# Kernel tuning notes

Measured on AMD Instinct MI355X. Metric: run time of the kernel, lower is better.

## Reference

```python
import jax, jax.numpy as jnp
import numpy as np

ROUTINGS = 3
NUM_CAPSULE = 32
DIM_CAPSULE = 64


def squash(x, axis=-1):
    # scale = sqrt(||x||^2 + eps) / (0.5 + ||x||^2 + eps)
    sq = jnp.sum(x * x, axis=axis, keepdims=True) + 1e-7
    return (jnp.sqrt(sq) / (0.5 + sq)) * x


def setup_inputs() -> dict:
    key = jax.random.key(0)
    k1, k2 = jax.random.split(key)
    B, IN, ID = 64, 1024, 256
    u_vecs = jax.random.normal(k1, (B, IN, ID), dtype=jnp.float32)
    # nn.Linear weight [NC*DC, ID], xavier_normal init
    fan_out, fan_in = NUM_CAPSULE * DIM_CAPSULE, ID
    std = np.sqrt(2.0 / (fan_in + fan_out)).astype(np.float32)
    W = jax.random.normal(k2, (fan_out, fan_in), dtype=jnp.float32) * std
    return {"u_vecs": u_vecs, "W": W}


def reference(u_vecs, W):
    B, IN, ID = u_vecs.shape
    # Linear projection: [B, IN, NC*DC]
    u_hat = jnp.einsum('bid,od->bio', u_vecs, W)
    # -> [B, NC, IN, DC]
    u_hat = u_hat.reshape(B, IN, NUM_CAPSULE, DIM_CAPSULE).transpose(0, 2, 1, 3)

    b = jnp.zeros((B, NUM_CAPSULE, IN), dtype=u_hat.dtype)
    o = None
    for i in range(ROUTINGS):
        c = jax.nn.softmax(b, axis=1)                      # softmax over output capsules
        o = jnp.einsum('bni,bnid->bnd', c, u_hat)          # [B, NC, DC]
        if i < ROUTINGS - 1:
            # F.normalize(o, 2, -1): x / max(||x||, 1e-12)
            norm = jnp.linalg.norm(o, axis=-1, keepdims=True)
            o = o / jnp.maximum(norm, 1e-12)
            b = jnp.einsum('bnid,bnd->bni', u_hat, o)
    return squash(o)
```

## Files before the change

### kernel.cpp

```cpp
#include <hip/hip_runtime.h>
#include <math.h>


#define B   64
#define IN  1024
#define ID  256
#define NC  32
#define DC  64

__global__ __launch_bounds__(256) void k_sumu(const float* __restrict__ u,
                                              float* __restrict__ sp0) {
    const int c = blockIdx.x, b = blockIdx.y;
    const int d = threadIdx.x;
    const float* up = u + ((size_t)b * IN + (size_t)c * (IN / 8)) * ID + d;
    float acc = 0.f;
#pragma unroll 8
    for (int i = 0; i < IN / 8; ++i) acc += up[(size_t)i * ID];
    sp0[(c * B + b) * ID + d] = acc;
}

__global__ __launch_bounds__(256) void k_ot(const float* __restrict__ W,
                                            const float* __restrict__ src,
                                            float* __restrict__ tout,
                                            const int mode) {
    const int bn = blockIdx.x;
    const int b = bn / NC, n = bn % NC;
    __shared__ float s_lds[ID];
    __shared__ float o_lds[DC];
    __shared__ float on_lds[DC];
    const int tid = threadIdx.x;

    float sv = 0.f;
    if (mode == 0) {
#pragma unroll
        for (int c = 0; c < 8; ++c) sv += src[(c * B + b) * ID + tid];
        sv *= (1.0f / NC);
    } else {
#pragma unroll
        for (int c = 0; c < 8; ++c) sv += src[((size_t)(c * B + b) * NC + n) * ID + tid];
    }
    s_lds[tid] = sv;
    __syncthreads();

    const int wave = tid >> 6, lane = tid & 63;
    const float* Wn = W + (size_t)n * DC * ID;
#pragma unroll 4
    for (int r = 0; r < 16; ++r) {
        const int d = wave * 16 + r;
        const float* wrow = Wn + (size_t)d * ID;
        float p = wrow[lane]        * s_lds[lane]
                + wrow[lane + 64]   * s_lds[lane + 64]
                + wrow[lane + 128]  * s_lds[lane + 128]
                + wrow[lane + 192]  * s_lds[lane + 192];
#pragma unroll
        for (int off = 32; off > 0; off >>= 1) p += __shfl_down(p, off);
        if (lane == 0) o_lds[d] = p;
    }
    __syncthreads();

    if (mode == 2) {
        if (tid < DC) {
            float v = o_lds[tid];
            float sq = v * v;
#pragma unroll
            for (int off = 32; off > 0; off >>= 1) sq += __shfl_down(sq, off);
            sq = __shfl(sq, 0) + 1e-7f;
            const float sc = sqrtf(sq) / (0.5f + sq);
            tout[(size_t)(b * NC + n) * DC + tid] = v * sc;
        }
        return;
    }

    if (tid < DC) {
        float v = o_lds[tid];
        float sq = v * v;
#pragma unroll
        for (int off = 32; off > 0; off >>= 1) sq += __shfl_down(sq, off);
        sq = __shfl(sq, 0);
        const float inv = 1.0f / fmaxf(sqrtf(sq), 1e-12f);
        on_lds[tid] = v * inv;
    }
    __syncthreads();

    float acc = 0.f;
    const float* wc = Wn + tid;
#pragma unroll 8
    for (int d = 0; d < DC; ++d) acc += wc[(size_t)d * ID] * on_lds[d];
    tout[((size_t)b * NC + n) * ID + tid] = acc;
}

#define RTILE 128
__global__ __launch_bounds__(512) void k_route(const float* __restrict__ u,
                                               const float* __restrict__ t,
                                               float* __restrict__ sp) {
    const int it = blockIdx.x, b = blockIdx.y;
    const int iBase = it * RTILE;
    __shared__ float Tc[16][36];
    __shared__ float Us[16][132];
    __shared__ float cl[RTILE][36];
    const int tid = threadIdx.x;

    const int q = tid >> 3;
    const int r = tid & 7;
    float acc[2][4] = {{0.f}};
    const float* ub = u + ((size_t)b * IN + iBase) * ID;
    const float* tb = t + (size_t)b * NC * ID;
    const int tn = tid >> 4, tk = tid & 15;

    for (int kc = 0; kc < ID / 16; ++kc) {
        __syncthreads();
        {
            const int i = tid >> 2, c4 = tid & 3;
            const float4 v = *(const float4*)(ub + (size_t)i * ID + kc * 16 + c4 * 4);
            Us[c4 * 4 + 0][i] = v.x;
            Us[c4 * 4 + 1][i] = v.y;
            Us[c4 * 4 + 2][i] = v.z;
            Us[c4 * 4 + 3][i] = v.w;
        }
        Tc[tk][tn] = tb[(size_t)tn * ID + kc * 16 + tk];
        __syncthreads();
#pragma unroll
        for (int k = 0; k < 16; ++k) {
            const float2 a2 = *(const float2*)&Us[k][q * 2];
            const float4 b4 = *(const float4*)&Tc[k][r * 4];
            const float av[2] = {a2.x, a2.y};
            const float bv[4] = {b4.x, b4.y, b4.z, b4.w};
#pragma unroll
            for (int ii = 0; ii < 2; ++ii)
#pragma unroll
                for (int jj = 0; jj < 4; ++jj) acc[ii][jj] += av[ii] * bv[jj];
        }
    }

#pragma unroll
    for (int ii = 0; ii < 2; ++ii)
        *(float4*)&cl[q * 2 + ii][r * 4] =
            make_float4(acc[ii][0], acc[ii][1], acc[ii][2], acc[ii][3]);
    __syncthreads();

    {
        const int i = tid >> 2, quad = tid & 3;
        float v[8];
#pragma unroll
        for (int j = 0; j < 8; ++j) v[j] = cl[i][quad * 8 + j];
        float mx = v[0];
#pragma unroll
        for (int j = 1; j < 8; ++j) mx = fmaxf(mx, v[j]);
        mx = fmaxf(mx, __shfl_xor(mx, 1));
        mx = fmaxf(mx, __shfl_xor(mx, 2));
        float sum = 0.f;
#pragma unroll
        for (int j = 0; j < 8; ++j) { v[j] = __expf(v[j] - mx); sum += v[j]; }
        sum += __shfl_xor(sum, 1);
        sum += __shfl_xor(sum, 2);
        const float inv = 1.0f / sum;
#pragma unroll
        for (int j = 0; j < 8; ++j) cl[i][quad * 8 + j] = v[j] * inv;
    }
    __syncthreads();

    const int d4 = tid & 63;
    const int ng = tid >> 6;
    float a2[4][4] = {{0.f}};
    const float* ur = ub + d4 * 4;
#pragma unroll 4
    for (int i = 0; i < RTILE; ++i) {
        const float4 uv = *(const float4*)(ur + (size_t)i * ID);
        const float4 c0 = *(const float4*)&cl[i][ng * 4];
        const float cv[4] = {c0.x, c0.y, c0.z, c0.w};
        const float uvv[4] = {uv.x, uv.y, uv.z, uv.w};
#pragma unroll
        for (int j = 0; j < 4; ++j)
#pragma unroll
            for (int x = 0; x < 4; ++x) a2[j][x] += cv[j] * uvv[x];
    }

    float* spb = sp + (size_t)(it * B + b) * NC * ID;
#pragma unroll
    for (int j = 0; j < 4; ++j) {
        const int n = ng * 4 + j;
        *(float4*)&spb[(size_t)n * ID + d4 * 4] =
            make_float4(a2[j][0], a2[j][1], a2[j][2], a2[j][3]);
    }
}

extern "C" void kernel_launch(void* const* d_in, const int* in_sizes, int n_in,
                              void* d_out, int out_size, void* d_ws, size_t ws_size,
                              hipStream_t stream) {
    const float* u = (const float*)d_in[0];
    const float* W = (const float*)d_in[1];
    float* out = (float*)d_out;

    float* ws  = (float*)d_ws;
    float* t   = ws;
    float* sp  = t + (size_t)B * NC * ID;
    float* sp0 = sp + (size_t)8 * B * NC * ID;

    k_sumu <<<dim3(8, B), dim3(256), 0, stream>>>(u, sp0);
    k_ot   <<<dim3(B * NC), dim3(256), 0, stream>>>(W, sp0, t, 0);
    k_route<<<dim3(IN / RTILE, B), dim3(512), 0, stream>>>(u, t, sp);
    k_ot   <<<dim3(B * NC), dim3(256), 0, stream>>>(W, sp, t, 1);
    k_route<<<dim3(IN / RTILE, B), dim3(512), 0, stream>>>(u, t, sp);
    k_ot   <<<dim3(B * NC), dim3(256), 0, stream>>>(W, sp, out, 2);
}
```

Measured before the change: 231.9 us.

## Stage full T in swizzled LDS and use 4x4 register tiles with split-K in k_route

The routing GEMM in k_route now loads the whole per-batch T matrix (32x256) into LDS once, with an XOR swizzle, instead of reloading a transposed 16-column slice every k-step. The u tile is stored row-major with float4 writes, which drops the scalar transpose scatter. Each thread now computes a 4x4 output tile over half of each k-chunk, and thread pairs combine their partial sums with a shuffle. The goal is fewer LDS stores and bank conflicts and more FMAs per LDS load. In exchange, LDS use grows (32 KB for T plus the shared scratch), which may limit occupancy despite the launch-bounds hint.

```diff
diff --git a/kernel.cpp b/kernel.cpp
--- a/kernel.cpp
+++ b/kernel.cpp
@@ -90,52 +90,74 @@
 }
 
 #define RTILE 128
-__global__ __launch_bounds__(512) void k_route(const float* __restrict__ u,
-                                               const float* __restrict__ t,
-                                               float* __restrict__ sp) {
+__global__ __launch_bounds__(512, 4) void k_route(const float* __restrict__ u,
+                                                  const float* __restrict__ t,
+                                                  float* __restrict__ sp) {
     const int it = blockIdx.x, b = blockIdx.y;
     const int iBase = it * RTILE;
-    __shared__ float Tc[16][36];
-    __shared__ float Us[16][132];
-    __shared__ float cl[RTILE][36];
+    __shared__ __align__(16) float Tst[NC][ID];
+    __shared__ __align__(16) float rest[RTILE * 36];
+    float (*Us2)[20] = (float(*)[20])rest;
+    float (*cl)[36]  = (float(*)[36])rest;
     const int tid = threadIdx.x;
 
-    const int q = tid >> 3;
-    const int r = tid & 7;
-    float acc[2][4] = {{0.f}};
     const float* ub = u + ((size_t)b * IN + iBase) * ID;
     const float* tb = t + (size_t)b * NC * ID;
-    const int tn = tid >> 4, tk = tid & 15;
+
+#pragma unroll
+    for (int rep = 0; rep < 4; ++rep) {
+        const int idx = tid + rep * 512;
+        const int n = idx >> 6, c4 = idx & 63;
+        const float4 v = *(const float4*)(tb + (size_t)n * ID + c4 * 4);
+        *(float4*)&Tst[n][(c4 * 4) ^ ((n >> 2) << 2)] = v;
+    }
+
+    const int s  = tid & 1;
+    const int r  = (tid >> 1) & 7;
+    const int q  = tid >> 4;
+    const int i0 = q * 4, n0 = r * 4;
+    const int rsw = r << 2;
+    const int si = tid >> 2, sc4 = tid & 3;
+    float acc[4][4] = {{0.f}};
 
     for (int kc = 0; kc < ID / 16; ++kc) {
         __syncthreads();
-        {
-            const int i = tid >> 2, c4 = tid & 3;
-            const float4 v = *(const float4*)(ub + (size_t)i * ID + kc * 16 + c4 * 4);
-            Us[c4 * 4 + 0][i] = v.x;
-            Us[c4 * 4 + 1][i] = v.y;
-            Us[c4 * 4 + 2][i] = v.z;
-            Us[c4 * 4 + 3][i] = v.w;
+        *(float4*)&Us2[si][sc4 * 4] =
+            *(const float4*)(ub + (size_t)si * ID + kc * 16 + sc4 * 4);
+        __syncthreads();
+#pragma unroll
+        for (int kk4 = 0; kk4 < 2; ++kk4) {
+            const int lk = s * 8 + kk4 * 4;
+            float4 a[4], bv[4];
+#pragma unroll
+            for (int ii = 0; ii < 4; ++ii) a[ii] = *(const float4*)&Us2[i0 + ii][lk];
+            const int bc = (kc * 16 + lk) ^ rsw;
+#pragma unroll
+            for (int jj = 0; jj < 4; ++jj) bv[jj] = *(const float4*)&Tst[n0 + jj][bc];
+#pragma unroll
+            for (int ii = 0; ii < 4; ++ii)
+#pragma unroll
+                for (int jj = 0; jj < 4; ++jj)
+                    acc[ii][jj] += a[ii].x * bv[jj].x + a[ii].y * bv[jj].y
+                                 + a[ii].z * bv[jj].z + a[ii].w * bv[jj].w;
         }
-        Tc[tk][tn] = tb[(size_t)tn * ID + kc * 16 + tk];
-        __syncthreads();
-#pragma unroll
-        for (int k = 0; k < 16; ++k) {
-            const float2 a2 = *(const float2*)&Us[k][q * 2];
-            const float4 b4 = *(const float4*)&Tc[k][r * 4];
-            const float av[2] = {a2.x, a2.y};
-            const float bv[4] = {b4.x, b4.y, b4.z, b4.w};
-#pragma unroll
-            for (int ii = 0; ii < 2; ++ii)
-#pragma unroll
-                for (int jj = 0; jj < 4; ++jj) acc[ii][jj] += av[ii] * bv[jj];
+    }
+#pragma unroll
+    for (int ii = 0; ii < 4; ++ii)
+#pragma unroll
+        for (int jj = 0; jj < 4; ++jj)
+            acc[ii][jj] += __shfl_xor(acc[ii][jj], 1);
+
+    __syncthreads();
+    {
+        const int iiBase = s * 2;
+#pragma unroll
+        for (int v = 0; v < 2; ++v) {
+            const int ii = iiBase + v;
+            *(float4*)&cl[i0 + ii][n0] =
+                make_float4(acc[ii][0], acc[ii][1], acc[ii][2], acc[ii][3]);
         }
     }
-
-#pragma unroll
-    for (int ii = 0; ii < 2; ++ii)
-        *(float4*)&cl[q * 2 + ii][r * 4] =
-            make_float4(acc[ii][0], acc[ii][1], acc[ii][2], acc[ii][3]);
     __syncthreads();
 
     {
```

Result: slower. 239.1 us (+3.1%).
